# Kernel tuning notes

Measured on AMD Instinct MI355X. Metric: run time of the kernel, lower is better.

Reference implementation:

```python
import jax, jax.numpy as jnp
import numpy as np

R = 16            # filter radius (init kwarg r)
EPS = 0.01        # regularizer (init kwarg eps)
B, H, W, C, K = 2, 1024, 1024, 3, 4


def _make_kernel():
    # Gaussian kernel with theta_alpha = r/4, center tap zeroed (as in source)
    x, y = np.mgrid[-R:R + 1, -R:R + 1]
    theta = R / 4.0
    k = np.exp(-0.5 * (x ** 2 + y ** 2) / theta ** 2).astype(np.float32)
    k[R, R] = 0.0
    return jnp.asarray(k)


def setup_inputs() -> dict:
    key = jax.random.key(0)
    k1, k2 = jax.random.split(key)
    I = jax.random.uniform(k1, (B, H, W, C), dtype=jnp.float32)
    p = jax.random.uniform(k2, (B, H, W, K), dtype=jnp.float32)
    return {"I": I, "p": p}


def _gaussian_filter(src, kfft):
    # FFT-based 'same' convolution with the (2R+1)^2 Gaussian kernel over (h, w).
    # src: [b, h, w, *trailing]; filtering applied independently per trailing channel.
    shp = src.shape
    b, h, w = shp[0], shp[1], shp[2]
    s = src.reshape(b, h, w, -1)
    s = jnp.pad(s, ((0, 0), (R, R), (R, R), (0, 0)))          # [b, h+2R, w+2R, c]
    sf = jnp.fft.rfft2(s, axes=(1, 2))
    d = jnp.fft.irfft2(sf * kfft[None, :, :, None], s=(h + 2 * R, w + 2 * R), axes=(1, 2))
    d = d[:, 2 * R:, 2 * R:, :]                               # crop back to [b, h, w, c]
    return d.reshape(shp)


def _guided_filter(I, p):
    b, h, w, c = I.shape
    k = _make_kernel()
    ext_k = jnp.pad(k, ((0, h - 1), (0, w - 1)))              # [h+2R, w+2R]
    kfft = jnp.fft.rfft2(ext_k)
    gf = lambda x: _gaussian_filter(x, kfft)

    N = gf(jnp.ones((1, h, w, 1), I.dtype))                   # normalization map
    mean_I = gf(I) / N                                        # [b,h,w,c]
    mean_p = gf(p) / N                                        # [b,h,w,k]
    # cov(I, p): [b,h,w,c,k]
    cov_Ip = gf(I[..., :, None] * p[..., None, :]) / N[..., None] \
        - mean_I[..., :, None] * mean_p[..., None, :]
    # var(I): [b,h,w,c,c]
    var_I = gf(I[..., :, None] * I[..., None, :]) / N[..., None] \
        - mean_I[..., :, None] * mean_I[..., None, :]
    A = var_I + EPS * jnp.eye(c, dtype=I.dtype)
    a = jnp.linalg.solve(A, cov_Ip)                           # == inv(A) @ cov_Ip, [b,h,w,c,k]
    b_ = mean_p[..., None] - jnp.einsum('bhwck,bhwc->bhwk', a, mean_I)[..., None]  # [b,h,w,k,1]
    mean_a = gf(a) / N[..., None]
    mean_b = gf(b_) / N[..., None]
    q = jnp.einsum('bhwck,bhwc->bhwk', mean_a, I)[..., None] + mean_b
    return q.reshape(p.shape)


def reference(I, p):
    return _guided_filter(I, p)
```

## Files before the change

### kernel.cpp

```cpp
#include <hip/hip_runtime.h>


#define HH 1024
#define WW 1024
#define HWSZ (HH * WW)
#define RR 16
#define NT 33
#define EPSF 0.01f

#define VBY 32
#define VROWS (VBY + 2 * RR)
#define VCOLS 256

typedef unsigned short u16;
typedef unsigned int u32;

__device__ constexpr float WG[NT] = {
  0.000335463f, 0.000883827f, 0.002187492f, 0.005086072f, 0.011108997f,
  0.022794173f, 0.043936928f, 0.079559512f, 0.135335283f, 0.216265076f,
  0.324652467f, 0.457833362f, 0.606530660f, 0.754839602f, 0.882496903f,
  0.969233234f, 1.0f,         0.969233234f, 0.882496903f, 0.754839602f,
  0.606530660f, 0.457833362f, 0.324652467f, 0.216265076f, 0.135335283f,
  0.079559512f, 0.043936928f, 0.022794173f, 0.011108997f, 0.005086072f,
  0.002187492f, 0.000883827f, 0.000335463f
};

__device__ constexpr float wg_sum() {
  float s = 0.0f;
  for (int i = 0; i < NT; ++i) s += WG[i];
  return s;
}

__device__ __forceinline__ u16 f2bf(float f) {
  u32 u = __float_as_uint(f);
  u += 0x7fffu + ((u >> 16) & 1u);
  return (u16)(u >> 16);
}
__device__ __forceinline__ float bf2f(u16 v) { return __uint_as_float(((u32)v) << 16); }

__device__ __forceinline__ float win_w(int u, int n) {
  constexpr float S = wg_sum();
  if (u >= RR && u < n - RR) return S;
  float w = 0.0f;
#pragma unroll
  for (int i = 0; i < NT; ++i) {
    const int uu = u - RR + i;
    if (uu >= 0 && uu < n) w += WG[i];
  }
  return w;
}

__global__ __launch_bounds__(256) void k_prod_hblur(const float* __restrict__ I,
                                                    const float* __restrict__ P,
                                                    u16* __restrict__ HB) {
  __shared__ float sI[3][288];
  __shared__ float sp[4][288];
  const int tid = threadIdx.x;
  const int y = blockIdx.y;
  const int x0 = blockIdx.x * 256;
  {
    const int base = (y * WW + (x0 - RR)) * 3;
    for (int idx = tid; idx < 288 * 3; idx += 256) {
      const int xi = idx / 3;
      const int c = idx - xi * 3;
      const int xx = x0 - RR + xi;
      sI[c][xi] = (xx >= 0 && xx < WW) ? I[base + idx] : 0.0f;
    }
  }
  {
    const int base = (y * WW + (x0 - RR)) * 4;
    for (int idx = tid; idx < 288 * 4; idx += 256) {
      const int xi = idx >> 2;
      const int c = idx & 3;
      const int xx = x0 - RR + xi;
      sp[c][xi] = (xx >= 0 && xx < WW) ? P[base + idx] : 0.0f;
    }
  }
  __syncthreads();

  float acc[25];
#pragma unroll
  for (int j = 0; j < 25; ++j) acc[j] = 0.0f;

#pragma unroll
  for (int dx = 0; dx < NT; ++dx) {
    const float w = WG[dx];
    const float i0 = sI[0][tid + dx], i1 = sI[1][tid + dx], i2 = sI[2][tid + dx];
    const float p0 = sp[0][tid + dx], p1 = sp[1][tid + dx];
    const float p2 = sp[2][tid + dx], p3 = sp[3][tid + dx];
    const float wi0 = w * i0, wi1 = w * i1, wi2 = w * i2;
    const float wp0 = w * p0, wp1 = w * p1, wp2 = w * p2, wp3 = w * p3;
    acc[0] += wi0; acc[1] += wi1; acc[2] += wi2;
    acc[3] += wp0; acc[4] += wp1; acc[5] += wp2; acc[6] += wp3;
    acc[7]  += i0 * wp0; acc[8]  += i0 * wp1; acc[9]  += i0 * wp2; acc[10] += i0 * wp3;
    acc[11] += i1 * wp0; acc[12] += i1 * wp1; acc[13] += i1 * wp2; acc[14] += i1 * wp3;
    acc[15] += i2 * wp0; acc[16] += i2 * wp1; acc[17] += i2 * wp2; acc[18] += i2 * wp3;
    acc[19] += wi0 * i0; acc[20] += wi0 * i1; acc[21] += wi0 * i2;
    acc[22] += wi1 * i1; acc[23] += wi1 * i2; acc[24] += wi2 * i2;
  }
  const int o = y * WW + x0 + tid;
#pragma unroll
  for (int ch = 0; ch < 25; ++ch) HB[ch * HWSZ + o] = f2bf(acc[ch]);
}

__global__ __launch_bounds__(256) void k_vblur25(const u16* __restrict__ HB,
                                                 u16* __restrict__ M) {
  __shared__ u16 s[VROWS][VCOLS];
  const int tid = threadIdx.x;
  const int ch = blockIdx.z;
  const int xb = blockIdx.x * VCOLS;
  const int y0 = blockIdx.y * VBY;
  const int x = xb + tid;

  {
    const u16* src = HB + (size_t)ch * HWSZ + xb;
    uint4 tmp[8];
#pragma unroll
    for (int it = 0; it < 8; ++it) {
      const int id = it * 256 + tid;
      const int row = id >> 5;
      const int cir = id & 31;
      const int gy = y0 - RR + row;
      uint4 v = make_uint4(0u, 0u, 0u, 0u);
      if (gy >= 0 && gy < HH)
        v = *reinterpret_cast<const uint4*>(src + (size_t)gy * WW + cir * 8);
      tmp[it] = v;
    }
#pragma unroll
    for (int it = 0; it < 8; ++it) {
      const int id = it * 256 + tid;
      const int row = id >> 5;
      const int cir = id & 31;
      *reinterpret_cast<uint4*>(&s[row][cir * 8]) = tmp[it];
    }
  }
  __syncthreads();

  u16* dst = M + (size_t)ch * HWSZ;

  for (int c = 0; c < 4; ++c) {
    float a[8];
#pragma unroll
    for (int t = 0; t < 8; ++t) a[t] = 0.0f;
#pragma unroll
    for (int r = 0; r < 40; ++r) {
      const float v = bf2f(s[8 * c + r][tid]);
#pragma unroll
      for (int t = 0; t < 8; ++t) {
        const int dy = r - t;
        if (dy >= 0 && dy < NT) a[t] += WG[dy] * v;
      }
    }
#pragma unroll
    for (int t = 0; t < 8; ++t) {
      const int y = y0 + 8 * c + t;
      dst[y * WW + x] = f2bf(a[t]);
    }
  }
}

__global__ __launch_bounds__(256) void k_solve(const u16* __restrict__ M,
                                               const float* __restrict__ I,
                                               const float* __restrict__ P,
                                               float* __restrict__ AB,
                                               float* __restrict__ S0) {
  const int i = blockIdx.x * 256 + threadIdx.x;
  const int y = i >> 10;
  const int x = i & 1023;
  const float invN = __builtin_amdgcn_rcpf(win_w(x, WW) * win_w(y, HH) - 1.0f);

  const float I0 = I[i * 3], I1 = I[i * 3 + 1], I2 = I[i * 3 + 2];
  float p[4];
#pragma unroll
  for (int k = 0; k < 4; ++k) p[k] = P[i * 4 + k];

  const float mI0 = (bf2f(M[i]) - I0) * invN;
  const float mI1 = (bf2f(M[HWSZ + i]) - I1) * invN;
  const float mI2 = (bf2f(M[2 * HWSZ + i]) - I2) * invN;
  float mp[4];
#pragma unroll
  for (int k = 0; k < 4; ++k) mp[k] = (bf2f(M[(3 + k) * HWSZ + i]) - p[k]) * invN;
  float cov[12];
#pragma unroll
  for (int k = 0; k < 4; ++k) {
    cov[k]     = (bf2f(M[(7 + k) * HWSZ + i])  - I0 * p[k]) * invN - mI0 * mp[k];
    cov[4 + k] = (bf2f(M[(11 + k) * HWSZ + i]) - I1 * p[k]) * invN - mI1 * mp[k];
    cov[8 + k] = (bf2f(M[(15 + k) * HWSZ + i]) - I2 * p[k]) * invN - mI2 * mp[k];
  }
  const float A00 = (bf2f(M[19 * HWSZ + i]) - I0 * I0) * invN - mI0 * mI0 + EPSF;
  const float A01 = (bf2f(M[20 * HWSZ + i]) - I0 * I1) * invN - mI0 * mI1;
  const float A02 = (bf2f(M[21 * HWSZ + i]) - I0 * I2) * invN - mI0 * mI2;
  const float A11 = (bf2f(M[22 * HWSZ + i]) - I1 * I1) * invN - mI1 * mI1 + EPSF;
  const float A12 = (bf2f(M[23 * HWSZ + i]) - I1 * I2) * invN - mI1 * mI2;
  const float A22 = (bf2f(M[24 * HWSZ + i]) - I2 * I2) * invN - mI2 * mI2 + EPSF;
  const float c00 = A11 * A22 - A12 * A12;
  const float c01 = A02 * A12 - A01 * A22;
  const float c02 = A01 * A12 - A02 * A11;
  const float det = A00 * c00 + A01 * c01 + A02 * c02;
  const float idet = 1.0f / det;
  const float i00 = c00 * idet, i01 = c01 * idet, i02 = c02 * idet;
  const float i11 = (A00 * A22 - A02 * A02) * idet;
  const float i12 = (A01 * A02 - A00 * A12) * idet;
  const float i22 = (A00 * A11 - A01 * A01) * idet;
  float4 s0;
  float* s0p = &s0.x;
#pragma unroll
  for (int k = 0; k < 4; ++k) {
    const float a0 = i00 * cov[k] + i01 * cov[4 + k] + i02 * cov[8 + k];
    const float a1 = i01 * cov[k] + i11 * cov[4 + k] + i12 * cov[8 + k];
    const float a2 = i02 * cov[k] + i12 * cov[4 + k] + i22 * cov[8 + k];
    const float b = mp[k] - (a0 * mI0 + a1 * mI1 + a2 * mI2);
    AB[k * HWSZ + i] = a0;
    AB[(4 + k) * HWSZ + i] = a1;
    AB[(8 + k) * HWSZ + i] = a2;
    AB[(12 + k) * HWSZ + i] = b;
    s0p[k] = a0 * I0 + a1 * I1 + a2 * I2 + b;
  }
  *reinterpret_cast<float4*>(S0 + (size_t)i * 4) = s0;
}

__global__ __launch_bounds__(256) void k_hblur16(const float* __restrict__ AB,
                                                 u16* __restrict__ HB) {
  __shared__ float s[1056];
  const int tid = threadIdx.x;
  const int y = blockIdx.x;
  const int ch = blockIdx.y;
  const float* src = AB + (size_t)ch * HWSZ + y * WW;
  if (tid < 16) { s[tid] = 0.0f; s[1040 + tid] = 0.0f; }
  *reinterpret_cast<float4*>(&s[16 + 4 * tid]) =
      *reinterpret_cast<const float4*>(&src[4 * tid]);
  __syncthreads();

  float vals[36];
  {
    const float4* s4 = reinterpret_cast<const float4*>(s) + tid;
#pragma unroll
    for (int r = 0; r < 9; ++r) {
      const float4 q = s4[r];
      vals[4 * r] = q.x; vals[4 * r + 1] = q.y;
      vals[4 * r + 2] = q.z; vals[4 * r + 3] = q.w;
    }
  }
  float acc[4] = {0.0f, 0.0f, 0.0f, 0.0f};
#pragma unroll
  for (int r = 0; r < 36; ++r) {
#pragma unroll
    for (int k = 0; k < 4; ++k) {
      const int dy = r - k;
      if (dy >= 0 && dy < NT) acc[k] += WG[dy] * vals[r];
    }
  }
  const u32 lo = (u32)f2bf(acc[0]) | ((u32)f2bf(acc[1]) << 16);
  const u32 hi = (u32)f2bf(acc[2]) | ((u32)f2bf(acc[3]) << 16);
  *reinterpret_cast<uint2*>(&HB[(size_t)ch * HWSZ + y * WW + 4 * tid]) =
      make_uint2(lo, hi);
}

__global__ __launch_bounds__(256) void k_vblur16(const u16* __restrict__ HB,
                                                 u16* __restrict__ MB) {
  __shared__ u16 s[VROWS][VCOLS];
  const int tid = threadIdx.x;
  const int ch = blockIdx.z;
  const int xb = blockIdx.x * VCOLS;
  const int y0 = blockIdx.y * VBY;
  const int x = xb + tid;

  {
    const u16* src = HB + (size_t)ch * HWSZ + xb;
    uint4 tmp[8];
#pragma unroll
    for (int it = 0; it < 8; ++it) {
      const int id = it * 256 + tid;
      const int row = id >> 5;
      const int cir = id & 31;
      const int gy = y0 - RR + row;
      uint4 v = make_uint4(0u, 0u, 0u, 0u);
      if (gy >= 0 && gy < HH)
        v = *reinterpret_cast<const uint4*>(src + (size_t)gy * WW + cir * 8);
      tmp[it] = v;
    }
#pragma unroll
    for (int it = 0; it < 8; ++it) {
      const int id = it * 256 + tid;
      const int row = id >> 5;
      const int cir = id & 31;
      *reinterpret_cast<uint4*>(&s[row][cir * 8]) = tmp[it];
    }
  }
  __syncthreads();

  u16* dst = MB + (size_t)ch * HWSZ;

  for (int c = 0; c < 4; ++c) {
    float a[8];
#pragma unroll
    for (int t = 0; t < 8; ++t) a[t] = 0.0f;
#pragma unroll
    for (int r = 0; r < 40; ++r) {
      const float v = bf2f(s[8 * c + r][tid]);
#pragma unroll
      for (int t = 0; t < 8; ++t) {
        const int dy = r - t;
        if (dy >= 0 && dy < NT) a[t] += WG[dy] * v;
      }
    }
#pragma unroll
    for (int t = 0; t < 8; ++t) {
      const int y = y0 + 8 * c + t;
      dst[y * WW + x] = f2bf(a[t]);
    }
  }
}

__global__ __launch_bounds__(256) void k_combine(const u16* __restrict__ MB,
                                                 const float* __restrict__ S0,
                                                 const float* __restrict__ I,
                                                 float* __restrict__ out) {
  const int i = blockIdx.x * 256 + threadIdx.x;
  const int y = i >> 10;
  const int x = i & 1023;
  const float invN = __builtin_amdgcn_rcpf(win_w(x, WW) * win_w(y, HH) - 1.0f);
  float m[16];
#pragma unroll
  for (int ch = 0; ch < 16; ++ch) m[ch] = bf2f(MB[(size_t)ch * HWSZ + i]);
  const float i0 = I[i * 3], i1 = I[i * 3 + 1], i2 = I[i * 3 + 2];
  const float4 s0 = *reinterpret_cast<const float4*>(S0 + (size_t)i * 4);
  float4 q;
  q.x = (m[0] * i0 + m[4] * i1 + m[8]  * i2 + m[12] - s0.x) * invN;
  q.y = (m[1] * i0 + m[5] * i1 + m[9]  * i2 + m[13] - s0.y) * invN;
  q.z = (m[2] * i0 + m[6] * i1 + m[10] * i2 + m[14] - s0.z) * invN;
  q.w = (m[3] * i0 + m[7] * i1 + m[11] * i2 + m[15] - s0.w) * invN;
  *reinterpret_cast<float4*>(out + (size_t)i * 4) = q;
}

extern "C" void kernel_launch(void* const* d_in, const int* in_sizes, int n_in,
                              void* d_out, int out_size, void* d_ws, size_t ws_size,
                              hipStream_t stream) {
  const float* I = (const float*)d_in[0];
  const float* P = (const float*)d_in[1];
  float* out = (float*)d_out;
  float* buf0 = (float*)d_ws;
  float* buf1 = buf0 + 25 * (size_t)HWSZ;

  u16* hb1 = (u16*)buf0;
  u16* Mb  = (u16*)buf1;
  float* AB = buf0;
  float* S0 = buf0 + 16 * (size_t)HWSZ;
  u16* hb2 = (u16*)buf1;
  u16* MBp = (u16*)buf1 + 16 * (size_t)HWSZ;

  for (int b = 0; b < 2; ++b) {
    const float* Ib = I + (size_t)b * HWSZ * 3;
    const float* Pb = P + (size_t)b * HWSZ * 4;
    float* outb = out + (size_t)b * HWSZ * 4;

    k_prod_hblur<<<dim3(WW / 256, HH), dim3(256), 0, stream>>>(Ib, Pb, hb1);
    k_vblur25<<<dim3(WW / VCOLS, HH / VBY, 25), dim3(256), 0, stream>>>(hb1, Mb);
    k_solve<<<dim3(HWSZ / 256), dim3(256), 0, stream>>>(Mb, Ib, Pb, AB, S0);
    k_hblur16<<<dim3(HH, 16), dim3(256), 0, stream>>>(AB, hb2);
    k_vblur16<<<dim3(WW / VCOLS, HH / VBY, 16), dim3(256), 0, stream>>>(hb2, MBp);
    k_combine<<<dim3(HWSZ / 256), dim3(256), 0, stream>>>(MBp, S0, Ib, outb);
  }
}
```

Before: 294.6 us.

## Compute four outputs per thread in product horizontal blur with full-row tiles

The product/horizontal-blur kernel now handles one full image row per block, and each thread produces four adjacent outputs. The 25 product channels are computed once per input position and scattered into four accumulator sets, instead of being recomputed for every tap of every output. Loads use float4 in both global and shared memory, and stores pack four bf16 values per channel. The cost is 100 accumulator registers per thread, which risks spills and lower occupancy, plus a grid of only 1024 blocks.

Result: slower. 327.3 us (+11.1%).

```diff
diff --git a/kernel.cpp b/kernel.cpp
--- a/kernel.cpp
+++ b/kernel.cpp
@@ -53,54 +53,97 @@
 __global__ __launch_bounds__(256) void k_prod_hblur(const float* __restrict__ I,
                                                     const float* __restrict__ P,
                                                     u16* __restrict__ HB) {
-  __shared__ float sI[3][288];
-  __shared__ float sp[4][288];
+  __shared__ float sI[3][1056];
+  __shared__ float sp[4][1056];
   const int tid = threadIdx.x;
-  const int y = blockIdx.y;
-  const int x0 = blockIdx.x * 256;
+  const int y = blockIdx.x;
+
   {
-    const int base = (y * WW + (x0 - RR)) * 3;
-    for (int idx = tid; idx < 288 * 3; idx += 256) {
-      const int xi = idx / 3;
-      const int c = idx - xi * 3;
-      const int xx = x0 - RR + xi;
-      sI[c][xi] = (xx >= 0 && xx < WW) ? I[base + idx] : 0.0f;
+    const float4* src = reinterpret_cast<const float4*>(I + (size_t)y * WW * 3);
+#pragma unroll
+    for (int it = 0; it < 3; ++it) {
+      const int id = it * 256 + tid;
+      const float4 v = src[id];
+      const float* vp = &v.x;
+      const int base = id * 4;
+#pragma unroll
+      for (int j = 0; j < 4; ++j) {
+        const int e = base + j;
+        const int x = e / 3;
+        const int c = e - 3 * x;
+        sI[c][16 + x] = vp[j];
+      }
     }
   }
   {
-    const int base = (y * WW + (x0 - RR)) * 4;
-    for (int idx = tid; idx < 288 * 4; idx += 256) {
-      const int xi = idx >> 2;
-      const int c = idx & 3;
-      const int xx = x0 - RR + xi;
-      sp[c][xi] = (xx >= 0 && xx < WW) ? P[base + idx] : 0.0f;
-    }
+    const float4* src = reinterpret_cast<const float4*>(P + (size_t)y * WW * 4);
+#pragma unroll
+    for (int it = 0; it < 4; ++it) {
+      const int x = it * 256 + tid;
+      const float4 v = src[x];
+      sp[0][16 + x] = v.x; sp[1][16 + x] = v.y;
+      sp[2][16 + x] = v.z; sp[3][16 + x] = v.w;
+    }
+  }
+  if (tid < 16) {
+#pragma unroll
+    for (int c = 0; c < 3; ++c) { sI[c][tid] = 0.0f; sI[c][1040 + tid] = 0.0f; }
+#pragma unroll
+    for (int c = 0; c < 4; ++c) { sp[c][tid] = 0.0f; sp[c][1040 + tid] = 0.0f; }
   }
   __syncthreads();
 
-  float acc[25];
-#pragma unroll
-  for (int j = 0; j < 25; ++j) acc[j] = 0.0f;
-
-#pragma unroll
-  for (int dx = 0; dx < NT; ++dx) {
-    const float w = WG[dx];
-    const float i0 = sI[0][tid + dx], i1 = sI[1][tid + dx], i2 = sI[2][tid + dx];
-    const float p0 = sp[0][tid + dx], p1 = sp[1][tid + dx];
-    const float p2 = sp[2][tid + dx], p3 = sp[3][tid + dx];
-    const float wi0 = w * i0, wi1 = w * i1, wi2 = w * i2;
-    const float wp0 = w * p0, wp1 = w * p1, wp2 = w * p2, wp3 = w * p3;
-    acc[0] += wi0; acc[1] += wi1; acc[2] += wi2;
-    acc[3] += wp0; acc[4] += wp1; acc[5] += wp2; acc[6] += wp3;
-    acc[7]  += i0 * wp0; acc[8]  += i0 * wp1; acc[9]  += i0 * wp2; acc[10] += i0 * wp3;
-    acc[11] += i1 * wp0; acc[12] += i1 * wp1; acc[13] += i1 * wp2; acc[14] += i1 * wp3;
-    acc[15] += i2 * wp0; acc[16] += i2 * wp1; acc[17] += i2 * wp2; acc[18] += i2 * wp3;
-    acc[19] += wi0 * i0; acc[20] += wi0 * i1; acc[21] += wi0 * i2;
-    acc[22] += wi1 * i1; acc[23] += wi1 * i2; acc[24] += wi2 * i2;
-  }
-  const int o = y * WW + x0 + tid;
-#pragma unroll
-  for (int ch = 0; ch < 25; ++ch) HB[ch * HWSZ + o] = f2bf(acc[ch]);
+  float acc[4][25];
+#pragma unroll
+  for (int k = 0; k < 4; ++k)
+#pragma unroll
+    for (int ch = 0; ch < 25; ++ch) acc[k][ch] = 0.0f;
+
+#pragma unroll
+  for (int r = 0; r < 9; ++r) {
+    float4 iv0, iv1, iv2, pv0, pv1, pv2, pv3;
+    iv0 = *reinterpret_cast<const float4*>(&sI[0][4 * tid + 4 * r]);
+    iv1 = *reinterpret_cast<const float4*>(&sI[1][4 * tid + 4 * r]);
+    iv2 = *reinterpret_cast<const float4*>(&sI[2][4 * tid + 4 * r]);
+    pv0 = *reinterpret_cast<const float4*>(&sp[0][4 * tid + 4 * r]);
+    pv1 = *reinterpret_cast<const float4*>(&sp[1][4 * tid + 4 * r]);
+    pv2 = *reinterpret_cast<const float4*>(&sp[2][4 * tid + 4 * r]);
+    pv3 = *reinterpret_cast<const float4*>(&sp[3][4 * tid + 4 * r]);
+    const float* i0p = &iv0.x; const float* i1p = &iv1.x; const float* i2p = &iv2.x;
+    const float* p0p = &pv0.x; const float* p1p = &pv1.x;
+    const float* p2p = &pv2.x; const float* p3p = &pv3.x;
+#pragma unroll
+    for (int j = 0; j < 4; ++j) {
+      const int pos = 4 * r + j;
+      const float i0 = i0p[j], i1 = i1p[j], i2 = i2p[j];
+      const float p0 = p0p[j], p1 = p1p[j], p2 = p2p[j], p3 = p3p[j];
+      float v[25];
+      v[0] = i0; v[1] = i1; v[2] = i2;
+      v[3] = p0; v[4] = p1; v[5] = p2; v[6] = p3;
+      v[7]  = i0 * p0; v[8]  = i0 * p1; v[9]  = i0 * p2; v[10] = i0 * p3;
+      v[11] = i1 * p0; v[12] = i1 * p1; v[13] = i1 * p2; v[14] = i1 * p3;
+      v[15] = i2 * p0; v[16] = i2 * p1; v[17] = i2 * p2; v[18] = i2 * p3;
+      v[19] = i0 * i0; v[20] = i0 * i1; v[21] = i0 * i2;
+      v[22] = i1 * i1; v[23] = i1 * i2; v[24] = i2 * i2;
+#pragma unroll
+      for (int k = 0; k < 4; ++k) {
+        const int dy = pos - k;
+        if (dy >= 0 && dy < NT) {
+          const float w = WG[dy];
+#pragma unroll
+          for (int ch = 0; ch < 25; ++ch) acc[k][ch] += w * v[ch];
+        }
+      }
+    }
+  }
+
+  const size_t o = (size_t)y * WW + 4 * tid;
+#pragma unroll
+  for (int ch = 0; ch < 25; ++ch) {
+    const u32 lo = (u32)f2bf(acc[0][ch]) | ((u32)f2bf(acc[1][ch]) << 16);
+    const u32 hi = (u32)f2bf(acc[2][ch]) | ((u32)f2bf(acc[3][ch]) << 16);
+    *reinterpret_cast<uint2*>(&HB[(size_t)ch * HWSZ + o]) = make_uint2(lo, hi);
+  }
 }
 
 __global__ __launch_bounds__(256) void k_vblur25(const u16* __restrict__ HB,
@@ -354,7 +397,7 @@
     const float* Pb = P + (size_t)b * HWSZ * 4;
     float* outb = out + (size_t)b * HWSZ * 4;
 
-    k_prod_hblur<<<dim3(WW / 256, HH), dim3(256), 0, stream>>>(Ib, Pb, hb1);
+    k_prod_hblur<<<dim3(HH), dim3(256), 0, stream>>>(Ib, Pb, hb1);
     k_vblur25<<<dim3(WW / VCOLS, HH / VBY, 25), dim3(256), 0, stream>>>(hb1, Mb);
     k_solve<<<dim3(HWSZ / 256), dim3(256), 0, stream>>>(Mb, Ib, Pb, AB, S0);
     k_hblur16<<<dim3(HH, 16), dim3(256), 0, stream>>>(AB, hb2);
```
